# Optimization experiments

Measured on AMD Instinct MI355X. Metric: run time of the kernel, lower is better.

## Reference

```python
import jax, jax.numpy as jnp
import numpy as np

NV, NDS, NF, HA, NC = 10475, 2048, 20908, 778, 500
INSIDE_W, OUTSIDE_W, CONTACT_W = 0.5, 2.0, 0.5
HCP_W, POSE_W, HANDPOSE_W, ANGLE_W = 1.0, 0.01, 0.01, 0.1
A1, A2, B1, B2 = 0.04, 0.04, 0.07, 0.06
C1, C2, D1, D2 = 0.01, 0.01, 0.023, 0.02


def setup_inputs() -> dict:
    key = jax.random.key(0)
    ks = jax.random.split(key, 16)
    vertices = jax.random.normal(ks[0], (1, NV, 3), dtype=jnp.float32)
    init_verts = vertices + 0.01 * jax.random.normal(ks[1], (1, NV, 3), dtype=jnp.float32)
    v2v_min = jax.random.uniform(ks[2], (NV,), dtype=jnp.float32) * 0.2
    v2v_min_idx = jax.random.randint(ks[3], (NV,), 0, NV, dtype=jnp.int32)
    ds = jnp.sort(jax.random.permutation(ks[4], NV)[:NDS]).astype(jnp.int32)  # unique downsample ids
    exterior = jax.random.randint(ks[5], (NDS,), 0, 2).astype(bool)
    geodist = jax.random.uniform(ks[6], (NV, NV), dtype=jnp.float32)
    init_verts_in_contact = jax.random.randint(ks[7], (NC,), 0, NV, dtype=jnp.int32)
    hand_contact_prior = jax.random.randint(ks[8], (2 * HA,), 0, NV, dtype=jnp.int32)
    hand_contact_prior_weights = jax.random.uniform(ks[9], (2 * HA,), dtype=jnp.float32)
    faces = jax.random.randint(ks[10], (NF, 3), 0, NV, dtype=jnp.int32)
    body_pose = 0.1 * jax.random.normal(ks[11], (1, 63), dtype=jnp.float32)
    init_pose = 0.1 * jax.random.normal(ks[12], (1, 63), dtype=jnp.float32)
    left_hand_pose = 0.1 * jax.random.normal(ks[13], (1, 45), dtype=jnp.float32)
    right_hand_pose = 0.1 * jax.random.normal(ks[14], (1, 45), dtype=jnp.float32)
    return dict(vertices=vertices, v2v_min=v2v_min, geodist=geodist,
                hand_contact_prior_weights=hand_contact_prior_weights,
                body_pose=body_pose, init_pose=init_pose,
                left_hand_pose=left_hand_pose, right_hand_pose=right_hand_pose,
                init_verts=init_verts, v2v_min_idx=v2v_min_idx, exterior=exterior,
                ds=ds, init_verts_in_contact=init_verts_in_contact,
                hand_contact_prior=hand_contact_prior, faces=faces)


def _masked_mean(x, m):
    s = jnp.sum(jnp.where(m, x, 0.0))
    c = jnp.sum(m)
    return jnp.where(c > 0, s / jnp.maximum(c, 1).astype(x.dtype), 0.0)


def _vertex_normals(verts, faces):
    # verts [NV,3], faces [NF,3] -> area-weighted vertex normals, normalized
    tris = verts[faces]                                   # [NF,3,3]
    fn = jnp.cross(tris[:, 1] - tris[:, 0], tris[:, 2] - tris[:, 0])  # [NF,3]
    vn = jnp.zeros_like(verts)
    vn = vn.at[faces[:, 0]].add(fn).at[faces[:, 1]].add(fn).at[faces[:, 2]].add(fn)
    return vn / (jnp.linalg.norm(vn, axis=-1, keepdims=True) + 1e-12)


def reference(vertices, v2v_min, geodist, hand_contact_prior_weights,
              body_pose, init_pose, left_hand_pose, right_hand_pose, init_verts,
              v2v_min_idx, exterior, ds, init_verts_in_contact, hand_contact_prior, faces):
    nv = vertices.shape[1]
    # inside mask: ds ids with ~exterior are inside (ds is unique)
    inside = jnp.zeros((nv,), dtype=bool).at[ds].set(~exterior)

    # ---- contact loss (attract exterior downsampled verts toward contact) ----
    gdi = jnp.min(geodist[:, init_verts_in_contact], axis=1)        # [NV] gather+min, memory-bound
    weights_outside = 1.0 / (5.0 * gdi + 1.0)
    m_out = ~inside[ds]
    v2voutside = A1 * weights_outside[ds] * jnp.tanh(v2v_min[ds] / A2)
    contactloss = CONTACT_W * _masked_mean(v2voutside, m_out)

    # ---- inside loss ----
    insideloss = INSIDE_W * _masked_mean(B1 * jnp.tanh(v2v_min / B2), inside)

    # ---- hand contact prior ----
    ha = hand_contact_prior.shape[0] // 2
    hvi = inside[hand_contact_prior]                                # [2*HA]
    lidx, ridx = hand_contact_prior[:ha], hand_contact_prior[ha:]
    lm_out, rm_out = ~hvi[:ha], ~hvi[ha:]
    lw = -0.1 * hand_contact_prior_weights[:ha] + 1.0
    rw = -0.1 * hand_contact_prior_weights[ha:] + 1.0
    l_out = C1 * jnp.tanh(v2v_min[lidx] / C2)
    r_out = C1 * jnp.tanh(v2v_min[ridx] / C2)
    hc_out = _masked_mean(lw * l_out, lm_out) + _masked_mean(rw * r_out, rm_out)
    l_in = D1 * jnp.tanh(v2v_min[lidx] / D2)
    r_in = D1 * jnp.tanh(v2v_min[ridx] / D2)
    hc_in = _masked_mean(l_in, hvi[:ha]) + _masked_mean(r_in, hvi[ha:])
    hand_contact_loss = HCP_W * (hc_in + hc_out)

    # ---- angle loss on close vertex pairs ----
    close = v2v_min < 0.01
    vn = _vertex_normals(vertices[0], faces)                        # [NV,3]
    # original mean over (i in all verts, j in close) of dot(n_i, n_{idx_j})
    nbar = jnp.mean(vn, axis=0)                                     # [3]
    ag = 1.0 + vn[v2v_min_idx] @ nbar                               # [NV]
    angle_loss = ANGLE_W * _masked_mean(ag, close)

    # ---- pose priors ----
    pose_prior_loss = POSE_W * jnp.sum((body_pose - init_pose) ** 2)
    hand_pose_prior_loss = HANDPOSE_W * (jnp.sum(left_hand_pose ** 2) + jnp.sum(right_hand_pose ** 2))

    # ---- outside (stay-close-to-init) loss, geodesic-weighted ----
    v2v0 = jnp.linalg.norm(init_verts - vertices, axis=2)           # [1,NV]
    gd = jnp.min(geodist[:, init_verts_in_contact], axis=1)         # [NV]
    w0 = (2.0 * gd.reshape(1, -1)) ** 2
    outsideloss = OUTSIDE_W * jnp.sum(v2v0 * w0)

    loss = (contactloss + insideloss + outsideloss + pose_prior_loss +
            hand_pose_prior_loss + angle_loss + hand_contact_loss)
    return loss
```

## Files before the change

kernel.cpp:

```cpp
#include <hip/hip_runtime.h>
#include <math.h>

#define INSIDE_W   0.5f
#define OUTSIDE_W  2.0f
#define CONTACT_W  0.5f
#define HCP_W      1.0f
#define POSE_W     0.01f
#define HANDPOSE_W 0.01f
#define ANGLE_W    0.1f
#define A1c 0.04f
#define A2c 0.04f
#define B1c 0.07f
#define B2c 0.06f
#define C1c 0.01f
#define C2c 0.01f
#define D1c 0.023f
#define D2c 0.02f

#define FBIG 3.402823e38f

__device__ __forceinline__ float waveReduceSum(float x) {
#pragma unroll
    for (int o = 32; o > 0; o >>= 1) x += __shfl_down(x, o, 64);
    return x;
}
__device__ __forceinline__ float waveReduceMin(float x) {
#pragma unroll
    for (int o = 32; o > 0; o >>= 1) x = fminf(x, __shfl_down(x, o, 64));
    return x;
}

__device__ __forceinline__ bool is_inside(int v, const int* __restrict__ ds,
                                          const int* __restrict__ ext, int NDS) {
    int lo = 0, hi = NDS - 1;
    while (lo <= hi) {
        int mid = (lo + hi) >> 1;
        int dv = ds[mid];
        if (dv == v) return ext[mid] == 0;
        if (dv < v) lo = mid + 1; else hi = mid - 1;
    }
    return false;
}


__global__ __launch_bounds__(256) void k_gdi(
    const float* __restrict__ geodist, const int* __restrict__ ivc,
    float* __restrict__ gdi, int NV, int NC)
{
    __shared__ int sivc[512];
    int v = blockIdx.x;
    const float* row = geodist + (size_t)v * (size_t)NV;
    for (int j = threadIdx.x; j < NC && j < 512; j += 256) sivc[j] = ivc[j];
    __syncthreads();
    float m = FBIG;
    for (int j = threadIdx.x; j < NC; j += 256) {
        int c = (j < 512) ? sivc[j] : ivc[j];
        m = fminf(m, row[c]);
    }
    m = waveReduceMin(m);
    __shared__ float sm[4];
    int lane = threadIdx.x & 63;
    int w = threadIdx.x >> 6;
    if (lane == 0) sm[w] = m;
    __syncthreads();
    if (threadIdx.x == 0)
        gdi[v] = fminf(fminf(sm[0], sm[1]), fminf(sm[2], sm[3]));
}

__global__ __launch_bounds__(256) void k_scatter(
    const float* __restrict__ verts, const int* __restrict__ faces,
    float* __restrict__ vn,
    const float* __restrict__ v2v_min, const int* __restrict__ v2v_min_idx,
    float* __restrict__ mf,
    const int* __restrict__ ds, const int* __restrict__ exterior,
    const int* __restrict__ hcp, const float* __restrict__ hcpw,
    float* __restrict__ accum,
    int NF, int NV, int NDS, int HA)
{
    int t = blockIdx.x * blockDim.x + threadIdx.x;
    if (t < NF) {
        int i0 = faces[t * 3 + 0];
        int i1 = faces[t * 3 + 1];
        int i2 = faces[t * 3 + 2];
        float p0x = verts[i0 * 3 + 0], p0y = verts[i0 * 3 + 1], p0z = verts[i0 * 3 + 2];
        float ax = verts[i1 * 3 + 0] - p0x;
        float ay = verts[i1 * 3 + 1] - p0y;
        float az = verts[i1 * 3 + 2] - p0z;
        float bx = verts[i2 * 3 + 0] - p0x;
        float by = verts[i2 * 3 + 1] - p0y;
        float bz = verts[i2 * 3 + 2] - p0z;
        float nx = ay * bz - az * by;
        float ny = az * bx - ax * bz;
        float nz = ax * by - ay * bx;
        atomicAdd(&vn[i0 * 3 + 0], nx);
        atomicAdd(&vn[i0 * 3 + 1], ny);
        atomicAdd(&vn[i0 * 3 + 2], nz);
        atomicAdd(&vn[i1 * 3 + 0], nx);
        atomicAdd(&vn[i1 * 3 + 1], ny);
        atomicAdd(&vn[i1 * 3 + 2], nz);
        atomicAdd(&vn[i2 * 3 + 0], nx);
        atomicAdd(&vn[i2 * 3 + 1], ny);
        atomicAdd(&vn[i2 * 3 + 2], nz);
    }
    float a[9];
#pragma unroll
    for (int k = 0; k < 9; ++k) a[k] = 0.f;
    if (t < NV) {
        if (v2v_min[t] < 0.01f) {
            atomicAdd(&mf[v2v_min_idx[t]], 1.0f);
            a[8] += 1.0f;
        }
    }
    if (t < HA) {
        int li = hcp[t];
        int ri = hcp[HA + t];
        float lw = 1.0f - 0.1f * hcpw[t];
        float rw = 1.0f - 0.1f * hcpw[HA + t];
        float lvm = v2v_min[li];
        float rvm = v2v_min[ri];
        if (is_inside(li, ds, exterior, NDS)) {
            a[4] += D1c * tanhf(lvm / D2c);
            a[5] += 1.0f;
        } else {
            a[0] += lw * C1c * tanhf(lvm / C2c);
            a[1] += 1.0f;
        }
        if (is_inside(ri, ds, exterior, NDS)) {
            a[6] += D1c * tanhf(rvm / D2c);
            a[7] += 1.0f;
        } else {
            a[2] += rw * C1c * tanhf(rvm / C2c);
            a[3] += 1.0f;
        }
    }
#pragma unroll
    for (int k = 0; k < 9; ++k) a[k] = waveReduceSum(a[k]);
    __shared__ float s[4][9];
    int lane = threadIdx.x & 63;
    int w = threadIdx.x >> 6;
    if (lane == 0) {
#pragma unroll
        for (int k = 0; k < 9; ++k) s[w][k] = a[k];
    }
    __syncthreads();
    if (threadIdx.x < 9) {
        float v = s[0][threadIdx.x] + s[1][threadIdx.x] + s[2][threadIdx.x] + s[3][threadIdx.x];
        if (v != 0.f) atomicAdd(&accum[threadIdx.x], v);
    }
}

__global__ __launch_bounds__(256) void k_normalize(
    float* __restrict__ vn, const float* __restrict__ mf,
    float* __restrict__ accum, int NV)
{
    int t = blockIdx.x * blockDim.x + threadIdx.x;
    float a[6] = {0.f, 0.f, 0.f, 0.f, 0.f, 0.f};
    if (t < NV) {
        float x = vn[t * 3 + 0];
        float y = vn[t * 3 + 1];
        float z = vn[t * 3 + 2];
        float inv = 1.0f / (sqrtf(x * x + y * y + z * z) + 1e-12f);
        x *= inv; y *= inv; z *= inv;
        vn[t * 3 + 0] = x;
        vn[t * 3 + 1] = y;
        vn[t * 3 + 2] = z;
        a[0] = x; a[1] = y; a[2] = z;
        float mm = mf[t];
        a[3] = mm * x; a[4] = mm * y; a[5] = mm * z;
    }
#pragma unroll
    for (int k = 0; k < 6; ++k) a[k] = waveReduceSum(a[k]);
    __shared__ float s[4][6];
    int lane = threadIdx.x & 63;
    int w = threadIdx.x >> 6;
    if (lane == 0) {
#pragma unroll
        for (int k = 0; k < 6; ++k) s[w][k] = a[k];
    }
    __syncthreads();
    if (threadIdx.x < 6) {
        float v = s[0][threadIdx.x] + s[1][threadIdx.x] + s[2][threadIdx.x] + s[3][threadIdx.x];
        if (v != 0.f) atomicAdd(&accum[9 + threadIdx.x], v);
    }
}

__global__ __launch_bounds__(1024) void k_final(
    const float* __restrict__ gdi,
    const float* __restrict__ verts, const float* __restrict__ iverts,
    const float* __restrict__ v2v_min,
    const int* __restrict__ ds, const int* __restrict__ exterior,
    const float* __restrict__ bp, const float* __restrict__ ip,
    const float* __restrict__ lh, const float* __restrict__ rh,
    const float* __restrict__ accum,
    float* __restrict__ out, int NV, int NDS)
{
    int tid = threadIdx.x;
    float outside = 0.f, cs = 0.f, cc = 0.f, ins = 0.f, inc = 0.f;
    float pose = 0.f, hand = 0.f;
    for (int t = tid; t < NV; t += 1024) {
        float g = gdi[t];
        float dx = iverts[t * 3 + 0] - verts[t * 3 + 0];
        float dy = iverts[t * 3 + 1] - verts[t * 3 + 1];
        float dz = iverts[t * 3 + 2] - verts[t * 3 + 2];
        float v2v0 = sqrtf(dx * dx + dy * dy + dz * dz);
        outside += v2v0 * 4.0f * g * g;
    }
    for (int j = tid; j < NDS; j += 1024) {
        int d = ds[j];
        float vm = v2v_min[d];
        if (exterior[j]) {
            float wo = 1.0f / (5.0f * gdi[d] + 1.0f);
            cs += A1c * wo * tanhf(vm / A2c);
            cc += 1.0f;
        } else {
            ins += B1c * tanhf(vm / B2c);
            inc += 1.0f;
        }
    }
    if (tid < 63) {
        float d = bp[tid] - ip[tid];
        pose = d * d;
    }
    if (tid < 45) {
        hand = lh[tid] * lh[tid] + rh[tid] * rh[tid];
    }
    float a[7] = {outside, cs, cc, ins, inc, pose, hand};
#pragma unroll
    for (int k = 0; k < 7; ++k) a[k] = waveReduceSum(a[k]);
    __shared__ float s[16][7];
    int lane = tid & 63;
    int w = tid >> 6;
    if (lane == 0) {
#pragma unroll
        for (int k = 0; k < 7; ++k) s[w][k] = a[k];
    }
    __syncthreads();
    if (tid == 0) {
        float r[7];
#pragma unroll
        for (int k = 0; k < 7; ++k) {
            float v = 0.f;
#pragma unroll
            for (int ww = 0; ww < 16; ++ww) v += s[ww][k];
            r[k] = v;
        }
        float lout_s = accum[0], lout_c = accum[1];
        float rout_s = accum[2], rout_c = accum[3];
        float lin_s  = accum[4], lin_c  = accum[5];
        float rin_s  = accum[6], rin_c  = accum[7];
        float close_c = accum[8];
        float nbx = accum[9]  / (float)NV;
        float nby = accum[10] / (float)NV;
        float nbz = accum[11] / (float)NV;
        float Sdot = accum[12] * nbx + accum[13] * nby + accum[14] * nbz;

        float contactloss = CONTACT_W * (r[2] > 0.f ? r[1] / r[2] : 0.f);
        float insideloss  = INSIDE_W  * (r[4] > 0.f ? r[3] / r[4] : 0.f);
        float hc_out = (lout_c > 0.f ? lout_s / lout_c : 0.f) + (rout_c > 0.f ? rout_s / rout_c : 0.f);
        float hc_in  = (lin_c  > 0.f ? lin_s  / lin_c  : 0.f) + (rin_c  > 0.f ? rin_s  / rin_c  : 0.f);
        float hand_contact_loss = HCP_W * (hc_in + hc_out);
        float angle_loss = ANGLE_W * (close_c > 0.f ? (close_c + Sdot) / close_c : 0.f);
        float outsideloss = OUTSIDE_W * r[0];
        float pose_prior_loss = POSE_W * r[5];
        float hand_pose_prior_loss = HANDPOSE_W * r[6];
        out[0] = contactloss + insideloss + outsideloss + pose_prior_loss +
                 hand_pose_prior_loss + angle_loss + hand_contact_loss;
    }
}

extern "C" void kernel_launch(void* const* d_in, const int* in_sizes, int n_in,
                              void* d_out, int out_size, void* d_ws, size_t ws_size,
                              hipStream_t stream)
{
    const float* verts    = (const float*)d_in[0];
    const float* v2v_min  = (const float*)d_in[1];
    const float* geodist  = (const float*)d_in[2];
    const float* hcpw     = (const float*)d_in[3];
    const float* bp       = (const float*)d_in[4];
    const float* ip       = (const float*)d_in[5];
    const float* lh       = (const float*)d_in[6];
    const float* rh       = (const float*)d_in[7];
    const float* iverts   = (const float*)d_in[8];
    const int*   vmi      = (const int*)d_in[9];
    const int*   exterior = (const int*)d_in[10];
    const int*   ds       = (const int*)d_in[11];
    const int*   ivc      = (const int*)d_in[12];
    const int*   hcp      = (const int*)d_in[13];
    const int*   faces    = (const int*)d_in[14];

    int NV  = in_sizes[1];
    int NDS = in_sizes[11];
    int NC  = in_sizes[12];
    int HA  = in_sizes[13] / 2;
    int NF  = in_sizes[14] / 3;

    float* accum = (float*)d_ws;
    float* vn    = accum + 32;
    float* mf    = vn + 3 * (size_t)NV;
    float* gdi   = mf + NV;

    size_t zbytes = (size_t)(32 + 4 * (size_t)NV) * sizeof(float);
    hipMemsetAsync(d_ws, 0, zbytes, stream);

    k_gdi<<<NV, 256, 0, stream>>>(geodist, ivc, gdi, NV, NC);

    int nmax = NF > NV ? NF : NV;
    k_scatter<<<(nmax + 255) / 256, 256, 0, stream>>>(
        verts, faces, vn, v2v_min, vmi, mf, ds, exterior, hcp, hcpw, accum,
        NF, NV, NDS, HA);

    k_normalize<<<(NV + 255) / 256, 256, 0, stream>>>(vn, mf, accum, NV);

    k_final<<<1, 1024, 0, stream>>>(gdi, verts, iverts, v2v_min, ds, exterior,
                                    bp, ip, lh, rh, accum, (float*)d_out, NV, NDS);
}
```

Measured before the change: 104.3 us.

## Stream geodist rows with a precomputed contact mask and fold final reductions into earlier kernels

The random per-row gather of contact columns from geodist is replaced by a coalesced, vectorised, nontemporal full-row scan. Non-contact columns are masked to +FLT_MAX via a precomputed mask buffer, with four shifted copies so row starts stay 16-byte aligned. The per-vertex outside term moves into k_normalize and the downsample contact/inside sums move into k_scatter, leaving k_final as a tiny scalar combine. This trades more raw bytes read and two extra small setup kernels for full memory coalescing and less serial single-block work.

```diff
diff --git a/kernel.cpp b/kernel.cpp
--- a/kernel.cpp
+++ b/kernel.cpp
@@ -19,6 +19,8 @@
 
 #define FBIG 3.402823e38f
 
+typedef float f32x4 __attribute__((ext_vector_type(4)));
+
 __device__ __forceinline__ float waveReduceSum(float x) {
 #pragma unroll
     for (int o = 32; o > 0; o >>= 1) x += __shfl_down(x, o, 64);
@@ -43,27 +45,59 @@
 }
 
 
-__global__ __launch_bounds__(256) void k_gdi(
-    const float* __restrict__ geodist, const int* __restrict__ ivc,
-    float* __restrict__ gdi, int NV, int NC)
-{
-    __shared__ int sivc[512];
+__global__ __launch_bounds__(256) void k_init_big4(float* __restrict__ big4, int n)
+{
+    int t = blockIdx.x * blockDim.x + threadIdx.x;
+    if (t < n) big4[t] = FBIG;
+}
+
+__global__ __launch_bounds__(256) void k_scatter_big4(
+    float* __restrict__ big4, const int* __restrict__ ivc, int NC, int NVPAD)
+{
+    int j = blockIdx.x * blockDim.x + threadIdx.x;
+    if (j < NC) {
+        int c = ivc[j];
+#pragma unroll
+        for (int p = 0; p < 4; ++p) {
+            if (c >= p) big4[(size_t)p * NVPAD + (c - p)] = -FBIG;
+        }
+    }
+}
+
+__global__ __launch_bounds__(256) void k_gdi_stream(
+    const float* __restrict__ geodist, const float* __restrict__ big4,
+    float* __restrict__ gdi, int NV, int NVPAD)
+{
     int v = blockIdx.x;
-    const float* row = geodist + (size_t)v * (size_t)NV;
-    for (int j = threadIdx.x; j < NC && j < 512; j += 256) sivc[j] = ivc[j];
-    __syncthreads();
+    size_t base = (size_t)v * (size_t)NV;
+    int s = (int)((4 - (base & 3)) & 3);
+    const float* row  = geodist + base;
+    const float* bigp = big4 + (size_t)s * (size_t)NVPAD;
+    int t = threadIdx.x;
     float m = FBIG;
-    for (int j = threadIdx.x; j < NC; j += 256) {
-        int c = (j < 512) ? sivc[j] : ivc[j];
-        m = fminf(m, row[c]);
-    }
+
+    if (t < s) m = fminf(m, fmaxf(row[t], big4[t]));
+
+    int nmain = (NV - s) >> 2;
+    for (int q = t; q < nmain; q += 256) {
+        f32x4 val = __builtin_nontemporal_load((const f32x4*)(row + s + 4 * q));
+        f32x4 bg  = *(const f32x4*)(bigp + 4 * q);
+        float m0 = fminf(fmaxf(val[0], bg[0]), fmaxf(val[1], bg[1]));
+        float m1 = fminf(fmaxf(val[2], bg[2]), fmaxf(val[3], bg[3]));
+        m = fminf(m, fminf(m0, m1));
+    }
+
+    int tailstart = s + 4 * nmain;
+    int ntail = NV - tailstart;
+    if (t < ntail) m = fminf(m, fmaxf(row[tailstart + t], big4[tailstart + t]));
+
     m = waveReduceMin(m);
     __shared__ float sm[4];
-    int lane = threadIdx.x & 63;
-    int w = threadIdx.x >> 6;
+    int lane = t & 63;
+    int w = t >> 6;
     if (lane == 0) sm[w] = m;
     __syncthreads();
-    if (threadIdx.x == 0)
+    if (t == 0)
         gdi[v] = fminf(fminf(sm[0], sm[1]), fminf(sm[2], sm[3]));
 }
 
@@ -71,7 +105,7 @@
     const float* __restrict__ verts, const int* __restrict__ faces,
     float* __restrict__ vn,
     const float* __restrict__ v2v_min, const int* __restrict__ v2v_min_idx,
-    float* __restrict__ mf,
+    float* __restrict__ mf, const float* __restrict__ gdi,
     const int* __restrict__ ds, const int* __restrict__ exterior,
     const int* __restrict__ hcp, const float* __restrict__ hcpw,
     float* __restrict__ accum,
@@ -102,9 +136,9 @@
         atomicAdd(&vn[i2 * 3 + 1], ny);
         atomicAdd(&vn[i2 * 3 + 2], nz);
     }
-    float a[9];
-#pragma unroll
-    for (int k = 0; k < 9; ++k) a[k] = 0.f;
+    float a[13];
+#pragma unroll
+    for (int k = 0; k < 13; ++k) a[k] = 0.f;
     if (t < NV) {
         if (v2v_min[t] < 0.01f) {
             atomicAdd(&mf[v2v_min_idx[t]], 1.0f);
@@ -133,28 +167,43 @@
             a[3] += 1.0f;
         }
     }
-#pragma unroll
-    for (int k = 0; k < 9; ++k) a[k] = waveReduceSum(a[k]);
-    __shared__ float s[4][9];
+    if (t < NDS) {
+        int d = ds[t];
+        float vm = v2v_min[d];
+        if (exterior[t]) {
+            float wo = 1.0f / (5.0f * gdi[d] + 1.0f);
+            a[9]  += A1c * wo * tanhf(vm / A2c);
+            a[10] += 1.0f;
+        } else {
+            a[11] += B1c * tanhf(vm / B2c);
+            a[12] += 1.0f;
+        }
+    }
+#pragma unroll
+    for (int k = 0; k < 13; ++k) a[k] = waveReduceSum(a[k]);
+    __shared__ float s[4][13];
     int lane = threadIdx.x & 63;
     int w = threadIdx.x >> 6;
     if (lane == 0) {
 #pragma unroll
-        for (int k = 0; k < 9; ++k) s[w][k] = a[k];
+        for (int k = 0; k < 13; ++k) s[w][k] = a[k];
     }
     __syncthreads();
-    if (threadIdx.x < 9) {
+    if (threadIdx.x < 13) {
         float v = s[0][threadIdx.x] + s[1][threadIdx.x] + s[2][threadIdx.x] + s[3][threadIdx.x];
-        if (v != 0.f) atomicAdd(&accum[threadIdx.x], v);
+        int slot = (threadIdx.x < 9) ? threadIdx.x : (16 + threadIdx.x - 9);
+        if (v != 0.f) atomicAdd(&accum[slot], v);
     }
 }
 
 __global__ __launch_bounds__(256) void k_normalize(
     float* __restrict__ vn, const float* __restrict__ mf,
+    const float* __restrict__ gdi,
+    const float* __restrict__ verts, const float* __restrict__ iverts,
     float* __restrict__ accum, int NV)
 {
     int t = blockIdx.x * blockDim.x + threadIdx.x;
-    float a[6] = {0.f, 0.f, 0.f, 0.f, 0.f, 0.f};
+    float a[7] = {0.f, 0.f, 0.f, 0.f, 0.f, 0.f, 0.f};
     if (t < NV) {
         float x = vn[t * 3 + 0];
         float y = vn[t * 3 + 1];
@@ -167,83 +216,54 @@
         a[0] = x; a[1] = y; a[2] = z;
         float mm = mf[t];
         a[3] = mm * x; a[4] = mm * y; a[5] = mm * z;
-    }
-#pragma unroll
-    for (int k = 0; k < 6; ++k) a[k] = waveReduceSum(a[k]);
-    __shared__ float s[4][6];
-    int lane = threadIdx.x & 63;
-    int w = threadIdx.x >> 6;
-    if (lane == 0) {
-#pragma unroll
-        for (int k = 0; k < 6; ++k) s[w][k] = a[k];
-    }
-    __syncthreads();
-    if (threadIdx.x < 6) {
-        float v = s[0][threadIdx.x] + s[1][threadIdx.x] + s[2][threadIdx.x] + s[3][threadIdx.x];
-        if (v != 0.f) atomicAdd(&accum[9 + threadIdx.x], v);
-    }
-}
-
-__global__ __launch_bounds__(1024) void k_final(
-    const float* __restrict__ gdi,
-    const float* __restrict__ verts, const float* __restrict__ iverts,
-    const float* __restrict__ v2v_min,
-    const int* __restrict__ ds, const int* __restrict__ exterior,
-    const float* __restrict__ bp, const float* __restrict__ ip,
-    const float* __restrict__ lh, const float* __restrict__ rh,
-    const float* __restrict__ accum,
-    float* __restrict__ out, int NV, int NDS)
-{
-    int tid = threadIdx.x;
-    float outside = 0.f, cs = 0.f, cc = 0.f, ins = 0.f, inc = 0.f;
-    float pose = 0.f, hand = 0.f;
-    for (int t = tid; t < NV; t += 1024) {
         float g = gdi[t];
         float dx = iverts[t * 3 + 0] - verts[t * 3 + 0];
         float dy = iverts[t * 3 + 1] - verts[t * 3 + 1];
         float dz = iverts[t * 3 + 2] - verts[t * 3 + 2];
         float v2v0 = sqrtf(dx * dx + dy * dy + dz * dz);
-        outside += v2v0 * 4.0f * g * g;
-    }
-    for (int j = tid; j < NDS; j += 1024) {
-        int d = ds[j];
-        float vm = v2v_min[d];
-        if (exterior[j]) {
-            float wo = 1.0f / (5.0f * gdi[d] + 1.0f);
-            cs += A1c * wo * tanhf(vm / A2c);
-            cc += 1.0f;
-        } else {
-            ins += B1c * tanhf(vm / B2c);
-            inc += 1.0f;
-        }
-    }
-    if (tid < 63) {
-        float d = bp[tid] - ip[tid];
+        a[6] = v2v0 * 4.0f * g * g;
+    }
+#pragma unroll
+    for (int k = 0; k < 7; ++k) a[k] = waveReduceSum(a[k]);
+    __shared__ float s[4][7];
+    int lane = threadIdx.x & 63;
+    int w = threadIdx.x >> 6;
+    if (lane == 0) {
+#pragma unroll
+        for (int k = 0; k < 7; ++k) s[w][k] = a[k];
+    }
+    __syncthreads();
+    if (threadIdx.x < 7) {
+        float v = s[0][threadIdx.x] + s[1][threadIdx.x] + s[2][threadIdx.x] + s[3][threadIdx.x];
+        if (v != 0.f) atomicAdd(&accum[9 + threadIdx.x], v);
+    }
+}
+
+__global__ __launch_bounds__(128) void k_final(
+    const float* __restrict__ accum,
+    const float* __restrict__ bp, const float* __restrict__ ip,
+    const float* __restrict__ lh, const float* __restrict__ rh,
+    float* __restrict__ out, int NV)
+{
+    int t = threadIdx.x;
+    float pose = 0.f, hand = 0.f;
+    if (t < 63) {
+        float d = bp[t] - ip[t];
         pose = d * d;
     }
-    if (tid < 45) {
-        hand = lh[tid] * lh[tid] + rh[tid] * rh[tid];
-    }
-    float a[7] = {outside, cs, cc, ins, inc, pose, hand};
-#pragma unroll
-    for (int k = 0; k < 7; ++k) a[k] = waveReduceSum(a[k]);
-    __shared__ float s[16][7];
-    int lane = tid & 63;
-    int w = tid >> 6;
-    if (lane == 0) {
-#pragma unroll
-        for (int k = 0; k < 7; ++k) s[w][k] = a[k];
-    }
+    if (t < 45) {
+        hand = lh[t] * lh[t] + rh[t] * rh[t];
+    }
+    pose = waveReduceSum(pose);
+    hand = waveReduceSum(hand);
+    __shared__ float s[2][2];
+    int lane = t & 63;
+    int w = t >> 6;
+    if (lane == 0) { s[w][0] = pose; s[w][1] = hand; }
     __syncthreads();
-    if (tid == 0) {
-        float r[7];
-#pragma unroll
-        for (int k = 0; k < 7; ++k) {
-            float v = 0.f;
-#pragma unroll
-            for (int ww = 0; ww < 16; ++ww) v += s[ww][k];
-            r[k] = v;
-        }
+    if (t == 0) {
+        pose = s[0][0] + s[1][0];
+        hand = s[0][1] + s[1][1];
         float lout_s = accum[0], lout_c = accum[1];
         float rout_s = accum[2], rout_c = accum[3];
         float lin_s  = accum[4], lin_c  = accum[5];
@@ -253,16 +273,19 @@
         float nby = accum[10] / (float)NV;
         float nbz = accum[11] / (float)NV;
         float Sdot = accum[12] * nbx + accum[13] * nby + accum[14] * nbz;
-
-        float contactloss = CONTACT_W * (r[2] > 0.f ? r[1] / r[2] : 0.f);
-        float insideloss  = INSIDE_W  * (r[4] > 0.f ? r[3] / r[4] : 0.f);
+        float outside_s = accum[15];
+        float contact_s = accum[16], contact_c = accum[17];
+        float inside_s  = accum[18], inside_c  = accum[19];
+
+        float contactloss = CONTACT_W * (contact_c > 0.f ? contact_s / contact_c : 0.f);
+        float insideloss  = INSIDE_W  * (inside_c  > 0.f ? inside_s  / inside_c  : 0.f);
         float hc_out = (lout_c > 0.f ? lout_s / lout_c : 0.f) + (rout_c > 0.f ? rout_s / rout_c : 0.f);
         float hc_in  = (lin_c  > 0.f ? lin_s  / lin_c  : 0.f) + (rin_c  > 0.f ? rin_s  / rin_c  : 0.f);
         float hand_contact_loss = HCP_W * (hc_in + hc_out);
         float angle_loss = ANGLE_W * (close_c > 0.f ? (close_c + Sdot) / close_c : 0.f);
-        float outsideloss = OUTSIDE_W * r[0];
-        float pose_prior_loss = POSE_W * r[5];
-        float hand_pose_prior_loss = HANDPOSE_W * r[6];
+        float outsideloss = OUTSIDE_W * outside_s;
+        float pose_prior_loss = POSE_W * pose;
+        float hand_pose_prior_loss = HANDPOSE_W * hand;
         out[0] = contactloss + insideloss + outsideloss + pose_prior_loss +
                  hand_pose_prior_loss + angle_loss + hand_contact_loss;
     }
@@ -294,23 +317,31 @@
     int HA  = in_sizes[13] / 2;
     int NF  = in_sizes[14] / 3;
 
+    int NVPAD = (NV + 15) & ~15;
+
     float* accum = (float*)d_ws;
     float* vn    = accum + 32;
     float* mf    = vn + 3 * (size_t)NV;
     float* gdi   = mf + NV;
+    size_t off = 32 + 5 * (size_t)NV;
+    off = (off + 3) & ~(size_t)3;
+    float* big4  = (float*)d_ws + off;
 
     size_t zbytes = (size_t)(32 + 4 * (size_t)NV) * sizeof(float);
     hipMemsetAsync(d_ws, 0, zbytes, stream);
 
-    k_gdi<<<NV, 256, 0, stream>>>(geodist, ivc, gdi, NV, NC);
+    int nbig = 4 * NVPAD;
+    k_init_big4<<<(nbig + 255) / 256, 256, 0, stream>>>(big4, nbig);
+    k_scatter_big4<<<(NC + 255) / 256, 256, 0, stream>>>(big4, ivc, NC, NVPAD);
+
+    k_gdi_stream<<<NV, 256, 0, stream>>>(geodist, big4, gdi, NV, NVPAD);
 
     int nmax = NF > NV ? NF : NV;
     k_scatter<<<(nmax + 255) / 256, 256, 0, stream>>>(
-        verts, faces, vn, v2v_min, vmi, mf, ds, exterior, hcp, hcpw, accum,
+        verts, faces, vn, v2v_min, vmi, mf, gdi, ds, exterior, hcp, hcpw, accum,
         NF, NV, NDS, HA);
 
-    k_normalize<<<(NV + 255) / 256, 256, 0, stream>>>(vn, mf, accum, NV);
-
-    k_final<<<1, 1024, 0, stream>>>(gdi, verts, iverts, v2v_min, ds, exterior,
-                                    bp, ip, lh, rh, accum, (float*)d_out, NV, NDS);
-}
+    k_normalize<<<(NV + 255) / 256, 256, 0, stream>>>(vn, mf, gdi, verts, iverts, accum, NV);
+
+    k_final<<<1, 128, 0, stream>>>(accum, bp, ip, lh, rh, (float*)d_out, NV);
+}
```

New measurement: 115.8 us. +11.0%, slower.
